# Optimization experiments

Measured on AMD Instinct MI355X. Metric: run time of the kernel, lower is better.

## Reference

```python
import jax, jax.numpy as jnp
import numpy as np

D_MODEL = 512
NUM_HEADS = 8
HEAD_DIM = D_MODEL // NUM_HEADS
BATCH = 4
SEQ = 2048
ROPE_BASE = 10000.0


def rope_cos_sin(seq_len, head_dim):
    inv_freq = 1.0 / (ROPE_BASE ** (jnp.arange(0, head_dim, 2, dtype=jnp.float32) / head_dim))
    t = jnp.arange(seq_len, dtype=jnp.float32)
    freqs = jnp.outer(t, inv_freq)              # (S, head_dim/2)
    emb = jnp.concatenate([freqs, freqs], axis=-1)  # (S, head_dim)
    return jnp.cos(emb), jnp.sin(emb)


def apply_rope(x, cos, sin):
    # x: (..., S, head_dim); cos/sin: (S, head_dim)
    x1 = x[..., ::2]
    x2 = x[..., 1::2]
    ch = cos[..., ::2]
    sh = sin[..., ::2]
    r1 = x1 * ch - x2 * sh
    r2 = x1 * sh + x2 * ch
    return jnp.stack([r1, r2], axis=-1).reshape(x.shape)


def setup_inputs() -> dict:
    key = jax.random.key(0)
    ks = jax.random.split(key, 12)
    x = jax.random.normal(ks[0], (BATCH, SEQ, D_MODEL), dtype=jnp.float32)
    variate_ids = jnp.sort(jax.random.randint(ks[1], (BATCH, SEQ), 0, 8), axis=-1).astype(jnp.int64)
    mask = jnp.ones((BATCH, SEQ), dtype=jnp.float32)
    s = 1.0 / np.sqrt(D_MODEL)
    Wq = jax.random.normal(ks[2], (D_MODEL, D_MODEL), dtype=jnp.float32) * s
    bq = jnp.zeros((D_MODEL,), dtype=jnp.float32)
    Wk = jax.random.normal(ks[3], (D_MODEL, D_MODEL), dtype=jnp.float32) * s
    bk = jnp.zeros((D_MODEL,), dtype=jnp.float32)
    Wv = jax.random.normal(ks[4], (D_MODEL, D_MODEL), dtype=jnp.float32) * s
    bv = jnp.zeros((D_MODEL,), dtype=jnp.float32)
    Wo = jax.random.normal(ks[5], (D_MODEL, D_MODEL), dtype=jnp.float32) * s
    bo = jnp.zeros((D_MODEL,), dtype=jnp.float32)
    u_same = jax.random.normal(ks[6], (NUM_HEADS,), dtype=jnp.float32) * 0.1
    u_cross = jax.random.normal(ks[7], (NUM_HEADS,), dtype=jnp.float32) * 0.1
    return dict(x=x, variate_ids=variate_ids, mask=mask, Wq=Wq, bq=bq, Wk=Wk, bk=bk,
                Wv=Wv, bv=bv, Wo=Wo, bo=bo, u_same=u_same, u_cross=u_cross)


def reference(x, variate_ids, mask, Wq, bq, Wk, bk, Wv, bv, Wo, bo, u_same, u_cross):
    B, S, D = x.shape
    H, Hd = NUM_HEADS, HEAD_DIM
    scale = 1.0 / np.sqrt(Hd)

    def proj(W, b):
        return (x @ W.T + b).reshape(B, S, H, Hd).transpose(0, 2, 1, 3)  # (B,H,S,Hd)

    q = proj(Wq, bq)
    k = proj(Wk, bk)
    v = proj(Wv, bv)

    cos, sin = rope_cos_sin(S, Hd)
    q = apply_rope(q, cos, sin)
    k = apply_rope(k, cos, sin)

    scores = jnp.einsum('bhid,bhjd->bhij', q, k) * scale  # (B,H,S,S)
    same = (variate_ids[:, :, None] == variate_ids[:, None, :]).astype(jnp.float32)  # (B,S,S)
    bias = same[:, None] * u_same[None, :, None, None] + (1.0 - same)[:, None] * u_cross[None, :, None, None]
    scores = scores + bias
    scores = scores + (1.0 - mask[:, None, None, :]) * -1e9
    probs = jax.nn.softmax(scores, axis=-1)
    out = jnp.einsum('bhij,bhjd->bhid', probs, v)  # (B,H,S,Hd)
    out = out.transpose(0, 2, 1, 3).reshape(B, S, D)
    return out @ Wo.T + bo
```

## Files before the change

kernel.cpp:

```cpp
#include <hip/hip_runtime.h>
#include <hip/hip_bf16.h>

#define BATCH   4
#define SEQ     2048
#define DMODEL  512
#define NHEADS  8
#define HEADDIM 64
#define MTOT    (BATCH*SEQ)
#define NX      (MTOT*DMODEL)
#define NW      (DMODEL*DMODEL)
#define QTILE   64
#define KTILE   32
#define NKT_G   32

#define LOG2E   1.4426950408889634f
#define SCL2    0.18033688011112042f
#define SHIFT   14.426950408889634f

typedef unsigned short u16;
typedef __bf16 bf16x8 __attribute__((ext_vector_type(8)));
typedef float  f32x4  __attribute__((ext_vector_type(4)));
typedef unsigned short u16x4 __attribute__((ext_vector_type(4)));
typedef unsigned u32x2 __attribute__((ext_vector_type(2)));

#define MFMA(a,b,c) __builtin_amdgcn_mfma_f32_16x16x32_bf16(a,b,c,0,0,0)

__device__ __forceinline__ u16 f2bf(float f) {
    unsigned u = __float_as_uint(f);
    u += 0x7FFFu + ((u >> 16) & 1u);
    return (u16)(u >> 16);
}
__device__ __forceinline__ unsigned pk_bf16(float a, float b) {
    union { __hip_bfloat162 h; unsigned u; } cv;
    cv.h = __float22bfloat162_rn(make_float2(a, b));
    return cv.u;
}
__device__ __forceinline__ void gll16(const void* g, void* l) {
    __builtin_amdgcn_global_load_lds((const __attribute__((address_space(1))) void*)g,
                                     (__attribute__((address_space(3))) void*)l, 16, 0, 0);
}
__device__ __forceinline__ void gll4(const void* g, void* l) {
    __builtin_amdgcn_global_load_lds((const __attribute__((address_space(1))) void*)g,
                                     (__attribute__((address_space(3))) void*)l, 4, 0, 0);
}

#define NCVT4 ((NX + 4*NW)/4)
__global__ __launch_bounds__(256) void cvt_rope_kernel(
    const float* __restrict__ x,
    const float* __restrict__ wq, const float* __restrict__ wk,
    const float* __restrict__ wv, const float* __restrict__ wo,
    u16* __restrict__ xbf,
    u16* __restrict__ wqbf, u16* __restrict__ wkbf,
    u16* __restrict__ wvbf, u16* __restrict__ wobf,
    float2* __restrict__ cst)
{
    int i4 = blockIdx.x * 256 + threadIdx.x;
    if (i4 < NCVT4) {
        int i = i4 * 4;
        const float* s; u16* d; int o;
        if (i < NX) { s = x; d = xbf; o = i; }
        else {
            int j = i - NX;
            int r = j >> 18;
            o = j & (NW - 1);
            s = (r == 0) ? wq : (r == 1) ? wk : (r == 2) ? wv : wo;
            d = (r == 0) ? wqbf : (r == 1) ? wkbf : (r == 2) ? wvbf : wobf;
        }
        float4 v = *(const float4*)(s + o);
        u16x4 u = { f2bf(v.x), f2bf(v.y), f2bf(v.z), f2bf(v.w) };
        *(u16x4*)(d + o) = u;
    } else {
        int r = i4 - NCVT4;
        if (r < SEQ * 32 / 4) {
            int idx = r * 4;
            int s  = idx >> 5;
            int p0 = idx & 31;
#pragma unroll
            for (int t = 0; t < 4; ++t) {
                int p = p0 + t;
                float inv = __expf(-0.5756462732485115f * (float)(p & 15));
                float ang = (float)s * inv;
                cst[idx + t] = make_float2(cosf(ang), sinf(ang));
            }
        }
    }
}

#define TP 136
__global__ __launch_bounds__(256) void qkv_kernel(
    const u16* __restrict__ x,
    const u16* __restrict__ Wq, const float* __restrict__ bq,
    const u16* __restrict__ Wk, const float* __restrict__ bk,
    const u16* __restrict__ Wv, const float* __restrict__ bv,
    const float* __restrict__ cstf,
    u16* __restrict__ qws, u16* __restrict__ kws, u16* __restrict__ vtws)
{
    __shared__ alignas(16) u16 smem[128 * TP];
    u16* As = smem;
    u16* Bs = smem + 8192;

    const int m0 = blockIdx.x * 128;
    const int n0 = blockIdx.y * 128;
    const int tid  = threadIdx.x;
    const int w    = tid >> 6;
    const int lane = tid & 63;
    const int quad = lane >> 4;
    const int l16  = lane & 15;
    const int wm = w & 1, wn = w >> 1;

    const int sec = n0 >> 9;
    const int oc0 = n0 & 511;
    const u16*   Wm = (sec == 0) ? Wq : (sec == 1 ? Wk : Wv);
    const float* bb = (sec == 0) ? bq : (sec == 1 ? bk : bv);

    const int xb = (sec < 2) ? wn : wm;
    const int wb = (sec < 2) ? wm : wn;

    f32x4 acc[4][4] = {};

    for (int kb = 0; kb < 8; ++kb) {
#pragma unroll
        for (int it = 0; it < 4; ++it) {
            const int s   = it * 256 + tid;
            const int row = s >> 3;
            const int cb  = s & 7;
            const int gcol = kb * 64 + (((cb ^ (row & 7))) << 3);
            gll16(x  + (m0  + row) * 512 + gcol, &As[s * 8]);
            gll16(Wm + (oc0 + row) * 512 + gcol, &Bs[s * 8]);
        }
        __syncthreads();

#pragma unroll
        for (int ks = 0; ks < 2; ++ks) {
            bf16x8 xf[4], wf[4];
#pragma unroll
            for (int t = 0; t < 4; ++t) {
                const int xrow = xb * 64 + t * 16 + l16;
                const int wrow = wb * 64 + t * 16 + l16;
                xf[t] = *(const bf16x8*)&As[xrow * 64 + (((ks * 4 + quad) ^ (xrow & 7)) << 3)];
                wf[t] = *(const bf16x8*)&Bs[wrow * 64 + (((ks * 4 + quad) ^ (wrow & 7)) << 3)];
            }
            if (sec < 2) {
#pragma unroll
                for (int tm = 0; tm < 4; ++tm)
#pragma unroll
                    for (int tn = 0; tn < 4; ++tn)
                        acc[tm][tn] = MFMA(wf[tm], xf[tn], acc[tm][tn]);
            } else {
#pragma unroll
                for (int tm = 0; tm < 4; ++tm)
#pragma unroll
                    for (int tn = 0; tn < 4; ++tn)
                        acc[tm][tn] = MFMA(xf[tm], wf[tn], acc[tm][tn]);
            }
        }
        __syncthreads();
    }

    if (sec < 2) {
#pragma unroll
        for (int tm = 0; tm < 4; ++tm) {
            const int dls = wm * 64 + tm * 16 + quad * 4;
            const float4 bv4 = *(const float4*)&bb[oc0 + dls];
            const int pbase = ((oc0 + dls) & 63) >> 1;
#pragma unroll
            for (int tn = 0; tn < 4; ++tn) {
                const int sl = wn * 64 + tn * 16 + l16;
                const int sg = (m0 + sl) & 2047;
                const float4 cs = *(const float4*)&cstf[sg * 64 + pbase * 2];
                const float v0 = acc[tm][tn][0] + bv4.x;
                const float v1 = acc[tm][tn][1] + bv4.y;
                const float v2 = acc[tm][tn][2] + bv4.z;
                const float v3 = acc[tm][tn][3] + bv4.w;
                const float r0 = v0 * cs.x - v1 * cs.y;
                const float r1 = v1 * cs.x + v0 * cs.y;
                const float r2 = v2 * cs.z - v3 * cs.w;
                const float r3 = v3 * cs.z + v2 * cs.w;
                u32x2 pv = { pk_bf16(r0, r1), pk_bf16(r2, r3) };
                *(u32x2*)&smem[sl * TP + dls] = pv;
            }
        }
        __syncthreads();
        u16* dst0 = (sec == 0) ? qws : kws;
#pragma unroll
        for (int i = 0; i < 8; ++i) {
            const int c   = i * 256 + tid;
            const int sl  = c >> 4;
            const int d8  = (c & 15) * 8;
            const int gcol = oc0 + d8;
            const int hh  = gcol >> 6;
            const int dh  = gcol & 63;
            const int sgl = m0 + sl;
            const int bi  = sgl >> 11;
            const int s   = sgl & 2047;
            u16* dst = dst0 + (size_t)(bi * NHEADS + hh) * (SEQ * HEADDIM)
                            + (size_t)s * HEADDIM + dh;
            *(bf16x8*)dst = *(const bf16x8*)&smem[sl * TP + d8];
        }
    } else {
#pragma unroll
        for (int tm = 0; tm < 4; ++tm) {
            const int row_l = wm * 64 + tm * 16 + quad * 4;
#pragma unroll
            for (int tn = 0; tn < 4; ++tn) {
                const int col_l = wn * 64 + tn * 16 + l16;
                const float bval = bb[oc0 + col_l];
                u32x2 pv = { pk_bf16(acc[tm][tn][0] + bval, acc[tm][tn][1] + bval),
                             pk_bf16(acc[tm][tn][2] + bval, acc[tm][tn][3] + bval) };
                *(u32x2*)&smem[col_l * TP + row_l] = pv;
            }
        }
        __syncthreads();
        const int bi  = m0 >> 11;
        const int sgb = m0 & 2047;
#pragma unroll
        for (int i = 0; i < 8; ++i) {
            const int c    = i * 256 + tid;
            const int col  = c >> 4;
            const int sc8  = (c & 15) * 8;
            const int gcol = oc0 + col;
            const int hh   = gcol >> 6;
            const int d    = gcol & 63;
            u16* dst = vtws + (size_t)(bi * NHEADS + hh) * (SEQ * HEADDIM)
                            + (size_t)d * SEQ + sgb + sc8;
            *(bf16x8*)dst = *(const bf16x8*)&smem[col * TP + sc8];
        }
    }
}

__global__ __launch_bounds__(512, 6) void attn_kernel(
    const u16* __restrict__ qws, const u16* __restrict__ kws,
    const u16* __restrict__ vtl,
    const int* __restrict__ vids, const float* __restrict__ mask,
    const float* __restrict__ u_same, const float* __restrict__ u_cross,
    u16* __restrict__ attn)
{
    __shared__ alignas(16) u16 smem[16384];
    __shared__ int   bidm[2][2][KTILE];
    __shared__ float bmkm[2][2][KTILE];
    __shared__ float comb_li2[2][QTILE];

    const int bh = blockIdx.y;
    const int b  = bh >> 3;
    const int h  = bh & 7;
    const int q0 = blockIdx.x * QTILE;

    const int tid  = threadIdx.x;
    const int w    = tid >> 6;
    const int lane = tid & 63;
    const int quad = lane >> 4;
    const int l16  = lane & 15;
    const int qw   = w & 3;
    const int kg   = w >> 2;
    const int tl   = tid & 255;

    const float us2 = u_same[h]  * LOG2E;
    const float uc2 = u_cross[h] * LOG2E;
    const size_t tb = (size_t)bh * (SEQ * HEADDIM);

    const int qr = q0 + qw * 16 + l16;
    const bf16x8 aq0 = *(const bf16x8*)(qws + tb + qr * HEADDIM + quad * 8);
    const bf16x8 aq1 = *(const bf16x8*)(qws + tb + qr * HEADDIM + 32 + quad * 8);

    const int vq = vids[b * SEQ + q0 + qw * 16 + l16];

    float li = 0.f;
    f32x4 o[4] = {};

    const int srow  = tl >> 3;
    const int scb   = tl & 7;
    const int soff  = ((scb ^ (srow & 7)) << 3);
    const int vrow  = tl >> 2;
    const int vcb   = (tl & 3) ^ ((vrow >> 1) & 3);
    const int soffv = (vcb << 3);
    const int kbase = kg * 2 * 2048;

    auto stage = [&](int t, int nb) {
        const int k0 = (kg * NKT_G + t) * KTILE;
        gll16(kws + tb + (size_t)(k0 + srow) * HEADDIM + soff,
              &smem[kbase + nb * 2048 + tl * 8]);
        gll16(vtl + tb + (size_t)vrow * SEQ + k0 + soffv,
              &smem[8192 + kbase + nb * 2048 + tl * 8]);
        if (tl < KTILE) {
            gll4(vids + b * SEQ + k0 + tl, &bidm[kg][nb][0]);
            gll4(mask + b * SEQ + k0 + tl, &bmkm[kg][nb][0]);
        }
    };

    auto body = [&](const int cur) {
        const u16* kb_b = &smem[kbase + cur * 2048];
        const u16* vb_b = &smem[8192 + kbase + cur * 2048];
        unsigned x0, x1, y0, y1;
#pragma unroll
        for (int nt = 0; nt < 2; ++nt) {
            const int krow = nt * 16 + l16;
            const int r7   = krow & 7;
            const bf16x8 kb0 = *(const bf16x8*)&kb_b[krow * 64 + ((quad ^ r7) << 3)];
            const bf16x8 kb1 = *(const bf16x8*)&kb_b[krow * 64 + ((quad ^ r7 ^ 4) << 3)];
            f32x4 sc = {};
            sc = MFMA(kb0, aq0, sc);
            sc = MFMA(kb1, aq1, sc);
            const int kk = nt * 16 + quad * 4;
            const int4   kv4 = *(const int4*)&bidm[kg][cur][kk];
            const float4 mk4 = *(const float4*)&bmkm[kg][cur][kk];
            const int   kvr[4] = { kv4.x, kv4.y, kv4.z, kv4.w };
            const float mkr[4] = { mk4.x, mk4.y, mk4.z, mk4.w };
            float p[4];
#pragma unroll
            for (int r = 0; r < 4; ++r) {
                const float mdl = fmaf(mkr[r], 1.4426950408889634e9f,
                                       -1.4426950408889634e9f - SHIFT);
                const float sel = (kvr[r] == vq) ? (us2 + mdl) : (uc2 + mdl);
                p[r] = __builtin_amdgcn_exp2f(fmaf(sc[r], SCL2, sel));
                li += p[r];
            }
            if (nt == 0) { x0 = pk_bf16(p[0], p[1]); x1 = pk_bf16(p[2], p[3]); }
            else         { y0 = pk_bf16(p[0], p[1]); y1 = pk_bf16(p[2], p[3]); }
        }

        const bool qlo = (quad < 2);
        const bool qod = (quad & 1);
        const unsigned a0 = qlo ? x0 : y0, a1 = qlo ? x1 : y1;
        const unsigned r0 = __shfl_xor((int)a0, 16), r1 = __shfl_xor((int)a1, 16);
        const unsigned b0 = qod ? x0 : y0, b1 = qod ? x1 : y1;
        const unsigned s0 = __shfl_xor((int)b0, 32), s1 = __shfl_xor((int)b1, 32);
        const unsigned c0 = qod ? y0 : x0, c1 = qod ? y1 : x1;
        const unsigned t0 = __shfl_xor((int)c0, 48), t1 = __shfl_xor((int)c1, 48);
        union { unsigned u[4]; bf16x8 v; } ap;
        ap.u[0] = (quad == 0) ? x0 : (quad == 1) ? t0 : (quad == 2) ? s0 : r0;
        ap.u[1] = (quad == 0) ? x1 : (quad == 1) ? t1 : (quad == 2) ? s1 : r1;
        ap.u[2] = (quad == 0) ? r0 : (quad == 1) ? s0 : (quad == 2) ? t0 : y0;
        ap.u[3] = (quad == 0) ? r1 : (quad == 1) ? s1 : (quad == 2) ? t1 : y1;

#pragma unroll
        for (int nt = 0; nt < 4; ++nt) {
            const int vr = nt * 16 + l16;
            const bf16x8 vb0 = *(const bf16x8*)&vb_b[vr * 32 + (((quad ^ ((vr >> 1) & 3))) << 3)];
            o[nt] = MFMA(ap.v, vb0, o[nt]);
        }
    };

    stage(0, 0);
    for (int t = 0; t < NKT_G; t += 2) {
        __syncthreads();
        stage(t + 1, 1);
        body(0);
        __syncthreads();
        if (t + 2 < NKT_G) stage(t + 2, 0);
        body(1);
    }

    float liq = li + __shfl_xor(li, 16);
    liq += __shfl_xor(liq, 32);
    __syncthreads();
    float* co = (float*)smem;
    if (quad == 0) comb_li2[kg][qw * 16 + l16] = liq;
    if (kg == 1) {
#pragma unroll
        for (int nt = 0; nt < 4; ++nt)
#pragma unroll
            for (int r = 0; r < 4; ++r)
                co[(qw * 16 + quad * 4 + r) * 65 + nt * 16 + l16] = o[nt][r];
    }
    __syncthreads();
    if (kg == 0) {
#pragma unroll
        for (int r = 0; r < 4; ++r) {
            const int qloc = qw * 16 + quad * 4 + r;
            const float lt = comb_li2[0][qloc] + comb_li2[1][qloc];
            const float inv = 1.0f / lt;
            const int R  = q0 + qloc;
            const int rb = (b * SEQ + R) * DMODEL + h * HEADDIM;
#pragma unroll
            for (int nt = 0; nt < 4; ++nt)
                attn[rb + nt * 16 + l16] =
                    f2bf((o[nt][r] + co[qloc * 65 + nt * 16 + l16]) * inv);
        }
    }
}

__global__ __launch_bounds__(256) void proj_kernel(
    const u16* __restrict__ a, const u16* __restrict__ Wo,
    const float* __restrict__ bo, float* __restrict__ out)
{
    __shared__ alignas(16) u16 psm[132 * 64 * 2];
    u16* As = psm;
    u16* Bs = psm + 8192;
    float* Lp = (float*)psm;

    const int m0 = blockIdx.x * 128;
    const int n0 = blockIdx.y * 128;
    const int tid  = threadIdx.x;
    const int w    = tid >> 6;
    const int lane = tid & 63;
    const int quad = lane >> 4;
    const int l16  = lane & 15;
    const int wm = w & 1, wn = w >> 1;

    f32x4 acc[4][4] = {};

    for (int kb = 0; kb < 8; ++kb) {
#pragma unroll
        for (int it = 0; it < 4; ++it) {
            const int s   = it * 256 + tid;
            const int row = s >> 3;
            const int cb  = s & 7;
            const int gcol = kb * 64 + (((cb ^ (row & 7))) << 3);
            gll16(a  + (m0 + row) * 512 + gcol, &As[s * 8]);
            gll16(Wo + (n0 + row) * 512 + gcol, &Bs[s * 8]);
        }
        __syncthreads();

#pragma unroll
        for (int ks = 0; ks < 2; ++ks) {
            bf16x8 af[4], wf[4];
#pragma unroll
            for (int t = 0; t < 4; ++t) {
                const int arow = wn * 64 + t * 16 + l16;
                const int wrow = wm * 64 + t * 16 + l16;
                af[t] = *(const bf16x8*)&As[arow * 64 + (((ks * 4 + quad) ^ (arow & 7)) << 3)];
                wf[t] = *(const bf16x8*)&Bs[wrow * 64 + (((ks * 4 + quad) ^ (wrow & 7)) << 3)];
            }
#pragma unroll
            for (int tm = 0; tm < 4; ++tm)
#pragma unroll
                for (int tn = 0; tn < 4; ++tn)
                    acc[tm][tn] = MFMA(wf[tm], af[tn], acc[tm][tn]);
        }
        __syncthreads();
    }

#pragma unroll
    for (int hph = 0; hph < 2; ++hph) {
        if (wn == hph) {
#pragma unroll
            for (int tm = 0; tm < 4; ++tm) {
                const int dls = wm * 64 + tm * 16 + quad * 4;
                const float4 bv4 = *(const float4*)&bo[n0 + dls];
#pragma unroll
                for (int tn = 0; tn < 4; ++tn) {
                    const int s2 = tn * 16 + l16;
                    float4 v = { acc[tm][tn][0] + bv4.x, acc[tm][tn][1] + bv4.y,
                                 acc[tm][tn][2] + bv4.z, acc[tm][tn][3] + bv4.w };
                    *(float4*)&Lp[s2 * 132 + dls] = v;
                }
            }
        }
        __syncthreads();
#pragma unroll
        for (int i = 0; i < 8; ++i) {
            const int c  = i * 256 + tid;
            const int s2 = c >> 5;
            const int dq = (c & 31) * 4;
            float4 v = *(const float4*)&Lp[s2 * 132 + dq];
            *(float4*)&out[(size_t)(m0 + hph * 64 + s2) * 512 + n0 + dq] = v;
        }
        __syncthreads();
    }
}

extern "C" void kernel_launch(void* const* d_in, const int* in_sizes, int n_in,
                              void* d_out, int out_size, void* d_ws, size_t ws_size,
                              hipStream_t stream) {
    const float* x    = (const float*)d_in[0];
    const int*   vids = (const int*)d_in[1];
    const float* mask = (const float*)d_in[2];
    const float* Wq = (const float*)d_in[3];
    const float* bq = (const float*)d_in[4];
    const float* Wk = (const float*)d_in[5];
    const float* bk = (const float*)d_in[6];
    const float* Wv = (const float*)d_in[7];
    const float* bv = (const float*)d_in[8];
    const float* Wo = (const float*)d_in[9];
    const float* bo = (const float*)d_in[10];
    const float* usame  = (const float*)d_in[11];
    const float* ucross = (const float*)d_in[12];
    float* out = (float*)d_out;

    u16* xbf  = (u16*)d_ws;
    u16* wqbf = xbf + NX;
    u16* wkbf = wqbf + NW;
    u16* wvbf = wkbf + NW;
    u16* wobf = wvbf + NW;
    float2* cst = (float2*)(wobf + NW);
    u16* qws  = (u16*)(cst + SEQ * 32);
    u16* kws  = qws + (size_t)BATCH * NHEADS * SEQ * HEADDIM;
    u16* vtws = kws + (size_t)BATCH * NHEADS * SEQ * HEADDIM;
    u16* attn = xbf;

    cvt_rope_kernel<<<(NCVT4 + SEQ * 32 / 4 + 255) / 256, 256, 0, stream>>>(
        x, Wq, Wk, Wv, Wo, xbf, wqbf, wkbf, wvbf, wobf, cst);

    dim3 g1(MTOT / 128, 3 * DMODEL / 128);
    qkv_kernel<<<g1, 256, 0, stream>>>(xbf, wqbf, bq, wkbf, bk, wvbf, bv,
                                       (const float*)cst, qws, kws, vtws);

    dim3 g2(SEQ / QTILE, BATCH * NHEADS);
    attn_kernel<<<g2, 512, 0, stream>>>(qws, kws, vtws, vids, mask,
                                        usame, ucross, attn);

    dim3 g3(MTOT / 128, DMODEL / 128);
    proj_kernel<<<g3, 256, 0, stream>>>(attn, wobf, bo, out);
}
```

Before: 207.5 us.

## Route P tile through per-wave LDS, remap blocks by XCD, simplify bias math

Replaces the cross-lane shuffle sequence that rearranged softmax probabilities into the MFMA A-operand layout with a per-wave LDS scratch buffer: each lane writes its packed bf16 probabilities and then reads back an 8-element row. It also remaps block IDs so that the four (batch, head) pairs sharing an XCD are grouped together, aiming for better L2 reuse of K/V, and folds the mask/bias constants into fewer ops. The LDS round trip costs extra shared memory and write/read latency in exchange for removing six shuffles and the select logic.

```diff
diff --git a/kernel.cpp b/kernel.cpp
--- a/kernel.cpp
+++ b/kernel.cpp
@@ -16,6 +16,7 @@
 #define LOG2E   1.4426950408889634f
 #define SCL2    0.18033688011112042f
 #define SHIFT   14.426950408889634f
+#define BIGL    1.4426950408889634e9f
 
 typedef unsigned short u16;
 typedef __bf16 bf16x8 __attribute__((ext_vector_type(8)));
@@ -236,14 +237,18 @@
     u16* __restrict__ attn)
 {
     __shared__ alignas(16) u16 smem[16384];
+    __shared__ alignas(16) u16 plsm[8 * 16 * 40];
     __shared__ int   bidm[2][2][KTILE];
     __shared__ float bmkm[2][2][KTILE];
     __shared__ float comb_li2[2][QTILE];
 
-    const int bh = blockIdx.y;
-    const int b  = bh >> 3;
-    const int h  = bh & 7;
-    const int q0 = blockIdx.x * QTILE;
+    const int id  = blockIdx.y * 32 + blockIdx.x;
+    const int xcd = id & 7;
+    const int idx = id >> 3;
+    const int bh  = xcd * 4 + (idx & 3);
+    const int q0  = (idx >> 2) * QTILE;
+    const int b   = bh >> 3;
+    const int h   = bh & 7;
 
     const int tid  = threadIdx.x;
     const int w    = tid >> 6;
@@ -256,6 +261,8 @@
 
     const float us2 = u_same[h]  * LOG2E;
     const float uc2 = u_cross[h] * LOG2E;
+    const float uc3 = uc2 - BIGL - SHIFT;
+    const float du2 = us2 - uc2;
     const size_t tb = (size_t)bh * (SEQ * HEADDIM);
 
     const int qr = q0 + qw * 16 + l16;
@@ -287,10 +294,11 @@
         }
     };
 
+    u16* const pw = &plsm[w * 640];
+
     auto body = [&](const int cur) {
         const u16* kb_b = &smem[kbase + cur * 2048];
         const u16* vb_b = &smem[8192 + kbase + cur * 2048];
-        unsigned x0, x1, y0, y1;
 #pragma unroll
         for (int nt = 0; nt < 2; ++nt) {
             const int krow = nt * 16 + l16;
@@ -308,35 +316,21 @@
             float p[4];
 #pragma unroll
             for (int r = 0; r < 4; ++r) {
-                const float mdl = fmaf(mkr[r], 1.4426950408889634e9f,
-                                       -1.4426950408889634e9f - SHIFT);
-                const float sel = (kvr[r] == vq) ? (us2 + mdl) : (uc2 + mdl);
+                const float sel = fmaf(mkr[r], BIGL, uc3) + ((kvr[r] == vq) ? du2 : 0.0f);
                 p[r] = __builtin_amdgcn_exp2f(fmaf(sc[r], SCL2, sel));
                 li += p[r];
             }
-            if (nt == 0) { x0 = pk_bf16(p[0], p[1]); x1 = pk_bf16(p[2], p[3]); }
-            else         { y0 = pk_bf16(p[0], p[1]); y1 = pk_bf16(p[2], p[3]); }
-        }
-
-        const bool qlo = (quad < 2);
-        const bool qod = (quad & 1);
-        const unsigned a0 = qlo ? x0 : y0, a1 = qlo ? x1 : y1;
-        const unsigned r0 = __shfl_xor((int)a0, 16), r1 = __shfl_xor((int)a1, 16);
-        const unsigned b0 = qod ? x0 : y0, b1 = qod ? x1 : y1;
-        const unsigned s0 = __shfl_xor((int)b0, 32), s1 = __shfl_xor((int)b1, 32);
-        const unsigned c0 = qod ? y0 : x0, c1 = qod ? y1 : x1;
-        const unsigned t0 = __shfl_xor((int)c0, 48), t1 = __shfl_xor((int)c1, 48);
-        union { unsigned u[4]; bf16x8 v; } ap;
-        ap.u[0] = (quad == 0) ? x0 : (quad == 1) ? t0 : (quad == 2) ? s0 : r0;
-        ap.u[1] = (quad == 0) ? x1 : (quad == 1) ? t1 : (quad == 2) ? s1 : r1;
-        ap.u[2] = (quad == 0) ? r0 : (quad == 1) ? s0 : (quad == 2) ? t0 : y0;
-        ap.u[3] = (quad == 0) ? r1 : (quad == 1) ? s1 : (quad == 2) ? t1 : y1;
+            u32x2 pv = { pk_bf16(p[0], p[1]), pk_bf16(p[2], p[3]) };
+            *(u32x2*)&pw[l16 * 40 + nt * 16 + quad * 4] = pv;
+        }
+
+        const bf16x8 ap = *(const bf16x8*)&pw[l16 * 40 + quad * 8];
 
 #pragma unroll
         for (int nt = 0; nt < 4; ++nt) {
             const int vr = nt * 16 + l16;
             const bf16x8 vb0 = *(const bf16x8*)&vb_b[vr * 32 + (((quad ^ ((vr >> 1) & 3))) << 3)];
-            o[nt] = MFMA(ap.v, vb0, o[nt]);
+            o[nt] = MFMA(ap, vb0, o[nt]);
         }
     };
 
```

Result: faster. 194.0 us (-6.5%).
